# Kernel optimization log

Measured on AMD Instinct MI355X. Metric: run time of the kernel, lower is better.

## Reference

```python
import jax, jax.numpy as jnp
from jax import lax
import numpy as np

B, S, V, C, H, Z, NSTEP = 256, 128, 128, 16, 1024, 256, 128
VC = V * C


def _gru_cell(x, h, Wih, Whh, bih, bhh):
    # torch GRUCell: gates ordered r, z, n along rows of (3H, in)
    gi = x @ Wih.T + bih
    gh = h @ Whh.T + bhh
    ir, iz, inn = jnp.split(gi, 3, axis=-1)
    hr, hz, hn = jnp.split(gh, 3, axis=-1)
    r = jax.nn.sigmoid(ir + hr)
    zg = jax.nn.sigmoid(iz + hz)
    n = jnp.tanh(inn + r * hn)
    return (1.0 - zg) * n + zg * h


def setup_inputs() -> dict:
    key = jax.random.key(0)
    ks = jax.random.split(key, 32)
    sc = 0.05
    p = lambda k, shape: (jax.random.normal(k, shape, jnp.float32) * sc)
    inp = {
        "x": jax.random.normal(ks[0], (B, V, S), jnp.float32),
        "noise": jax.random.normal(ks[1], (B, Z), jnp.float32),
        "gruf_Wih": p(ks[2], (3 * H, V)), "gruf_Whh": p(ks[3], (3 * H, H)),
        "gruf_bih": p(ks[4], (3 * H,)), "gruf_bhh": p(ks[5], (3 * H,)),
        "grub_Wih": p(ks[6], (3 * H, V)), "grub_Whh": p(ks[7], (3 * H, H)),
        "grub_bih": p(ks[8], (3 * H,)), "grub_bhh": p(ks[9], (3 * H,)),
        "Wmu": p(ks[10], (Z, 2 * H)), "bmu": p(ks[11], (Z,)),
        "Wvar": p(ks[12], (Z, 2 * H)), "bvar": p(ks[13], (Z,)),
        "Winit": p(ks[14], (H, Z)), "binit": p(ks[15], (H,)),
        "c1_Wih": p(ks[16], (3 * H, Z + VC)), "c1_Whh": p(ks[17], (3 * H, H)),
        "c1_bih": p(ks[18], (3 * H,)), "c1_bhh": p(ks[19], (3 * H,)),
        "c2_Wih": p(ks[20], (3 * H, H)), "c2_Whh": p(ks[21], (3 * H, H)),
        "c2_bih": p(ks[22], (3 * H,)), "c2_bhh": p(ks[23], (3 * H,)),
        "Wout": p(ks[24], (VC, H)), "bout": p(ks[25], (VC,)),
    }
    return inp


def reference(x, noise, gruf_Wih, gruf_Whh, gruf_bih, gruf_bhh,
              grub_Wih, grub_Whh, grub_bih, grub_bhh,
              Wmu, bmu, Wvar, bvar, Winit, binit,
              c1_Wih, c1_Whh, c1_bih, c1_bhh,
              c2_Wih, c2_Whh, c2_bih, c2_bhh, Wout, bout):
    b = x.shape[0]
    xe = jnp.transpose(x, (0, 2, 1))           # (b, s, V)
    xt = jnp.swapaxes(xe, 0, 1)                # (s, b, V) time-major
    h0 = jnp.zeros((b, H), x.dtype)

    def step_f(h, xs):
        h2 = _gru_cell(xs, h, gruf_Wih, gruf_Whh, gruf_bih, gruf_bhh)
        return h2, None

    def step_b(h, xs):
        h2 = _gru_cell(xs, h, grub_Wih, grub_Whh, grub_bih, grub_bhh)
        return h2, None

    hf, _ = lax.scan(step_f, h0, xt)
    hb, _ = lax.scan(step_b, h0, xt[::-1])
    enc = jnp.concatenate([hf, hb], axis=-1)   # (b, 2H) = h_n transposed+flattened

    mu = enc @ Wmu.T + bmu
    var = jnp.exp(enc @ Wvar.T + bvar)         # Normal(mu, var): var is the scale
    z = mu + var * noise                       # rsample

    out0 = jnp.zeros((b, VC), x.dtype).at[:, -1].set(1.0)
    h1_0 = jnp.tanh(z @ Winit.T + binit)
    h2_0 = jnp.zeros((b, H), x.dtype)

    def dstep(carry, i):
        out, h1, h2 = carry
        inp = jnp.concatenate([out, z], axis=1)          # (b, VC + Z)
        h1n = _gru_cell(inp, h1, c1_Wih, c1_Whh, c1_bih, c1_bhh)
        h2_prev = jnp.where(i == 0, h1n, h2)             # hx[1] = hx[0] at step 0
        h2n = _gru_cell(h1n, h2_prev, c2_Wih, c2_Whh, c2_bih, c2_bhh)
        logits = h2n @ Wout.T + bout                     # (b, VC)
        ls = jax.nn.log_softmax(logits.reshape(b, C, V), axis=1).reshape(b, VC)
        # eval-mode _sampling: argmax -> one-hot (no gradient flows through it)
        out_n = jax.nn.one_hot(jnp.argmax(ls, axis=1), VC, dtype=ls.dtype)
        return (out_n, h1n, h2n), ls

    _, xs = lax.scan(dstep, (out0, h1_0, h2_0), jnp.arange(NSTEP))
    recon_seq = jnp.swapaxes(xs, 0, 1)                   # (b, n_step, VC)
    recon = jnp.transpose(recon_seq, (0, 2, 1)).reshape(b, C, V, NSTEP)
    return mu, var, z, recon
```

## Files before the change

kernel.cpp:

```cpp
#include <hip/hip_runtime.h>
#include <cstdint>
#include <cstddef>

typedef __attribute__((ext_vector_type(8))) short bf16x8;
typedef __attribute__((ext_vector_type(4))) float f32x4;
#define DEVI __device__ __forceinline__

constexpr int B = 256, S = 128, V = 128, C = 16, H = 1024, Z = 256, NSTEP = 128;
constexpr int VC = V * C, G3 = 3 * H;
constexpr size_t BVC = (size_t)B * VC;

typedef __attribute__((address_space(1))) const unsigned short* gas_p;
typedef __attribute__((address_space(3))) unsigned short* las_p;

DEVI unsigned short f2bf(float f){unsigned u=__float_as_uint(f);u+=0x7fffu+((u>>16)&1u);return (unsigned short)(u>>16);}
DEVI float sigm(float x){return 1.f/(1.f+expf(-x));}
DEVI f32x4 MFMA(bf16x8 a,bf16x8 b,f32x4 c){return __builtin_amdgcn_mfma_f32_16x16x32_bf16(a,b,c,0,0,0);}
DEVI void stage16(const unsigned short* g, unsigned short* l){__builtin_amdgcn_global_load_lds((gas_p)g,(las_p)l,16,0,0);}

DEVI unsigned long long ldc8(const void* p){return __hip_atomic_load((const unsigned long long*)p,__ATOMIC_RELAXED,__HIP_MEMORY_SCOPE_AGENT);}
DEVI void stc8(void* p, unsigned long long v){__hip_atomic_store((unsigned long long*)p,v,__ATOMIC_RELAXED,__HIP_MEMORY_SCOPE_AGENT);}
DEVI unsigned ldc4(const void* p){return __hip_atomic_load((const unsigned*)p,__ATOMIC_RELAXED,__HIP_MEMORY_SCOPE_AGENT);}
DEVI void stc4(void* p, unsigned v){__hip_atomic_store((unsigned*)p,v,__ATOMIC_RELAXED,__HIP_MEMORY_SCOPE_AGENT);}
DEVI bf16x8 ldfragc(const unsigned short* p){
  union{bf16x8 v;unsigned long long q[2];}u;
  u.q[0]=ldc8(p); u.q[1]=ldc8(p+4); return u.v;
}
DEVI unsigned long long pack4(float a,float b,float c,float d){
  return (unsigned long long)f2bf(a)|((unsigned long long)f2bf(b)<<16)|((unsigned long long)f2bf(c)<<32)|((unsigned long long)f2bf(d)<<48);
}
DEVI unsigned long long packf2(float a,float b){
  return (unsigned long long)__float_as_uint(a)|((unsigned long long)__float_as_uint(b)<<32);
}

DEVI void wv(int n){
  if(n==0)      asm volatile("s_waitcnt vmcnt(0)":::"memory");
  else if(n==4) asm volatile("s_waitcnt vmcnt(4)":::"memory");
  else if(n==8) asm volatile("s_waitcnt vmcnt(8)":::"memory");
  else if(n==10)asm volatile("s_waitcnt vmcnt(10)":::"memory");
  else if(n==12)asm volatile("s_waitcnt vmcnt(12)":::"memory");
  else if(n==16)asm volatile("s_waitcnt vmcnt(16)":::"memory");
  else if(n==20)asm volatile("s_waitcnt vmcnt(20)":::"memory");
}
DEVI void lg0(){asm volatile("s_waitcnt lgkmcnt(0)":::"memory");}
DEVI void cmb(){asm volatile("" ::: "memory");}
DEVI void drain_sync(){asm volatile("s_waitcnt vmcnt(0) lgkmcnt(0)":::"memory");__syncthreads();}

DEVI void waitflags(const unsigned* f,int base,int n,unsigned tgt){
  int lane=threadIdx.x&63;
  if (lane<n){
    const unsigned* a=&f[(size_t)(base+lane)<<4];
    while (ldc4(a)<tgt) __builtin_amdgcn_s_sleep(2);
  }
}
DEVI unsigned waitseq(const unsigned* f,int base,int n,unsigned tgt){
  int lane=threadIdx.x&63; unsigned v=tgt<<16;
  if (lane<n){
    const unsigned* a=&f[(size_t)(base+lane)<<4];
    v=ldc4(a);
    while ((v>>16)<tgt){__builtin_amdgcn_s_sleep(2); v=ldc4(a);}
  }
  return v;
}

#define LDHD(SRC,KT,Ha,Hb) { (Ha)=ldfragc((SRC)+(size_t)mrow*H+((KT)<<6)+(l4<<3)); (Hb)=ldfragc((SRC)+(size_t)mrow*H+((KT)<<6)+((4+l4)<<3)); cmb(); }

__global__ void k_cvt(const float* __restrict__ src, unsigned short* __restrict__ dst, int n){
  for (int i=blockIdx.x*256+threadIdx.x;i<n;i+=gridDim.x*256) dst[i]=f2bf(src[i]);
}

__global__ void k_xt(const float* __restrict__ x, unsigned short* __restrict__ xtb){
  __shared__ float tile[32][33];
  int sb=blockIdx.x*32, rb=blockIdx.y*32, tx=threadIdx.x, ty=threadIdx.y;
  for (int i=ty;i<32;i+=8) tile[i][tx]=x[(size_t)(rb+i)*S+sb+tx];
  __syncthreads();
  for (int i=ty;i<32;i+=8) xtb[(size_t)(sb+i)*(B*V)+rb+tx]=f2bf(tile[tx][i]);
}

__global__ void k_wt(const float* __restrict__ w, float* __restrict__ wt){
  __shared__ float tile[32][33];
  int vb=blockIdx.x*32, nb=blockIdx.y*32, tx=threadIdx.x, ty=threadIdx.y;
  for (int i=ty;i<32;i+=8) tile[i][tx]=w[(size_t)(nb+i)*(VC+Z)+vb+tx];
  __syncthreads();
  for (int i=ty;i<32;i+=8) wt[(size_t)(vb+i)*G3+nb+tx]=tile[tx][i];
}

__global__ __launch_bounds__(256) void k_mu_var_z(const float* __restrict__ hf,const float* __restrict__ hb,
    const float* __restrict__ Wmu,const float* __restrict__ bmu,
    const float* __restrict__ Wvar,const float* __restrict__ bvar,
    const float* __restrict__ noise,
    float* __restrict__ omu,float* __restrict__ ovar,float* __restrict__ oz,float* __restrict__ zws){
  __shared__ float e[2*H];
  int b=blockIdx.x, t=threadIdx.x;
  for (int i=0;i<2*H/256;++i){int k=t+i*256; e[k]=(k<H)?hf[b*H+k]:hb[b*H+k-H];}
  __syncthreads();
  const float* wm=Wmu+(size_t)t*2*H; const float* wv2=Wvar+(size_t)t*2*H;
  float am=bmu[t], av=bvar[t];
  for (int k=0;k<2*H;++k){am+=e[k]*wm[k];av+=e[k]*wv2[k];}
  float vv=expf(av), zz=am+vv*noise[b*Z+t];
  omu[b*Z+t]=am; ovar[b*Z+t]=vv; oz[b*Z+t]=zz; zws[b*Z+t]=zz;
}

__global__ void k_zpart(const float* __restrict__ z,const float* __restrict__ c1Wih,
                        const float* __restrict__ bih,float* __restrict__ zpart){
  int idx=blockIdx.x*256+threadIdx.x;
  int b=idx/G3, n=idx%G3;
  const float* w=c1Wih+(size_t)n*(VC+Z)+VC;
  const float* zr=z+b*Z;
  float a=bih[n];
  for (int k=0;k<Z;++k) a+=zr[k]*w[k];
  zpart[idx]=a;
}

__global__ void k_h1init(const float* __restrict__ z,const float* __restrict__ Winit,
                         const float* __restrict__ binit,
                         float* __restrict__ h1f,unsigned short* __restrict__ h1b,unsigned* __restrict__ F4){
  int idx=blockIdx.x*256+threadIdx.x;
  int b=idx>>10, jj=idx&(H-1);
  const float* w=Winit+(size_t)jj*Z;
  const float* zr=z+b*Z;
  float a=binit[jj];
  for (int k=0;k<Z;++k) a+=zr[k]*w[k];
  float t=tanhf(a);
  h1f[idx]=t; h1b[idx]=f2bf(t);
  if (idx<B) F4[(size_t)idx<<4]=(unsigned)(VC-1);
}

struct EncP {
  const unsigned short *xtb,*wihf,*whhf,*wihb,*whhb;
  const float *bihf,*bhhf,*bihb,*bhhb;
  unsigned short *hf0,*hf1,*hb0,*hb1;
  float *hf,*hb;
  unsigned* FE;
};

#define ENC_MM(DB,H0,H1) { const unsigned short* bb=lw+(DB)*6144; \
  _Pragma("unroll") for (int kf=0;kf<2;++kf){ \
    const int sw=(((kf<<2)+l4)^(l15&7))<<3; \
    bf16x8 hh=kf?(H1):(H0); \
    _Pragma("unroll") for (int nj=0;nj<2;++nj){ \
      const int ro=((nj<<4)+l15)*64+sw; \
      bf16x8 w0=*(const bf16x8*)&bb[ro]; \
      bf16x8 w1=*(const bf16x8*)&bb[2048+ro]; \
      bf16x8 w2=*(const bf16x8*)&bb[4096+ro]; \
      aR[nj]=MFMA(w0,hh,aR[nj]); aZ[nj]=MFMA(w1,hh,aZ[nj]); aNH[nj]=MFMA(w2,hh,aNH[nj]); } } }

#define ENC_MMX(DB,XKT) { const unsigned short* bb=lw+(DB)*6144; \
  _Pragma("unroll") for (int kf=0;kf<2;++kf){ \
    const int ch=(kf<<2)+l4; const int sw=(ch^(l15&7))<<3; \
    bf16x8 hh=*(const bf16x8*)&P.xtb[(size_t)xs*(B*V)+(size_t)mrow*V+((XKT)<<6)+(ch<<3)]; \
    _Pragma("unroll") for (int nj=0;nj<2;++nj){ \
      const int ro=((nj<<4)+l15)*64+sw; \
      bf16x8 w0=*(const bf16x8*)&bb[ro]; \
      bf16x8 w1=*(const bf16x8*)&bb[2048+ro]; \
      bf16x8 w2=*(const bf16x8*)&bb[4096+ro]; \
      aR[nj]=MFMA(w0,hh,aR[nj]); aZ[nj]=MFMA(w1,hh,aZ[nj]); aNX[nj]=MFMA(w2,hh,aNX[nj]); } } }

__global__ __launch_bounds__(256,1) void k_enc(EncP P){
  __shared__ unsigned short lws[49152];
  const int tid=threadIdx.x, wave=tid>>6, lane=tid&63;
  const int l15=lane&15, l4=lane>>4, l8r=lane>>3, l8c=lane&7;
  const int bid=blockIdx.x, xcd=bid&7, q=bid>>3;
  const int dir=q>>4, q2=q&15, jt=(q2&1)*8+xcd, mt=q2>>1;
  const int wm=(wave&1)*16, wn=(wave>>1)*32;
  const int gbase=(bid>>4)<<4;
  const unsigned short* wih=dir?P.wihb:P.wihf;
  const unsigned short* whh=dir?P.whhb:P.whhf;
  const float* bih=dir?P.bihb:P.bihf;
  const float* bhh=dir?P.bhhb:P.bhhf;
  unsigned short* hbuf[2]={dir?P.hb0:P.hf0, dir?P.hb1:P.hf1};
  unsigned short* lw=&lws[wave*12288];
  const int mrow=mt*32+wm+l15;

  f32x4 biR[2],biZ[2],biN[2],bhR[2],bhZ[2],bhN[2];
#pragma unroll
  for (int nj=0;nj<2;++nj){
    int j0=jt*64+wn+nj*16+(l4<<2);
    biR[nj]=*(const f32x4*)&bih[j0]; biZ[nj]=*(const f32x4*)&bih[H+j0]; biN[nj]=*(const f32x4*)&bih[2*H+j0];
    bhR[nj]=*(const f32x4*)&bhh[j0]; bhZ[nj]=*(const f32x4*)&bhh[H+j0]; bhN[nj]=*(const f32x4*)&bhh[2*H+j0];
  }
  float hreg[2][4]={};

  auto Wh=[&](int kt,int db){
    unsigned short* d=lw+db*6144;
#pragma unroll
    for (int g=0;g<3;++g)
#pragma unroll
      for (int i=0;i<4;++i)
        stage16(whh+(size_t)((g<<10)+jt*64+wn+i*8+l8r)*H+(kt<<6)+((l8c^l8r)<<3), d+(g*32+i*8)*64);
    cmb();
  };
  auto Wx=[&](int kt,int db){
    unsigned short* d=lw+db*6144;
#pragma unroll
    for (int g=0;g<3;++g)
#pragma unroll
      for (int i=0;i<4;++i)
        stage16(wih+(size_t)((g<<10)+jt*64+wn+i*8+l8r)*V+(kt<<6)+((l8c^l8r)<<3), d+(g*32+i*8)*64);
    cmb();
  };

  Wh(0,0); Wh(1,1);

  for (int s=0;s<S;++s){
    waitflags(P.FE,gbase,16,(unsigned)s);
    const unsigned short* hsrc=hbuf[s&1];
    unsigned short* hdst=hbuf[(s+1)&1];
    const int xs=dir?(S-1-s):s;
    bf16x8 hA0,hA1,hB0,hB1;
    f32x4 aR[2]={},aZ[2]={},aNH[2]={},aNX[2]={};
    LDHD(hsrc,0,hA0,hA1); LDHD(hsrc,1,hB0,hB1);
    wv(4);  ENC_MM(0,hA0,hA1); lg0(); Wh(2,0); LDHD(hsrc,2,hA0,hA1);
    for (int i=0;i<6;++i){
      wv(16); ENC_MM(1,hB0,hB1); lg0(); Wh(2*i+3,1); LDHD(hsrc,2*i+3,hB0,hB1);
      wv(16); ENC_MM(0,hA0,hA1); lg0(); Wh(2*i+4,0); LDHD(hsrc,2*i+4,hA0,hA1);
    }
    wv(16); ENC_MM(1,hB0,hB1); lg0(); Wh(15,1); LDHD(hsrc,15,hB0,hB1);
    wv(16); ENC_MM(0,hA0,hA1); lg0(); Wx(0,0);
    wv(12); ENC_MM(1,hB0,hB1); lg0(); Wx(1,1);
    wv(12); ENC_MMX(0,0); lg0();
    wv(0);  ENC_MMX(1,1); lg0();
#pragma unroll
    for (int nj=0;nj<2;++nj){
      int j0=jt*64+wn+nj*16+(l4<<2);
      float hv[4];
#pragma unroll
      for (int r=0;r<4;++r){
        float rg=sigm(aR[nj][r]+biR[nj][r]+bhR[nj][r]);
        float zg=sigm(aZ[nj][r]+biZ[nj][r]+bhZ[nj][r]);
        float nn=tanhf(aNX[nj][r]+biN[nj][r]+rg*(aNH[nj][r]+bhN[nj][r]));
        float hnew=(1.f-zg)*nn+zg*hreg[nj][r];
        hreg[nj][r]=hnew; hv[r]=hnew;
      }
      stc8(hdst+(size_t)mrow*H+j0, pack4(hv[0],hv[1],hv[2],hv[3]));
    }
    drain_sync();
    if (tid==0) stc4(&P.FE[(size_t)bid<<4],(unsigned)(s+1));
    Wh(0,0); Wh(1,1);
  }
  float* hout=dir?P.hb:P.hf;
#pragma unroll
  for (int nj=0;nj<2;++nj){
    int j0=jt*64+wn+nj*16+(l4<<2);
    f32x4 v; v[0]=hreg[nj][0];v[1]=hreg[nj][1];v[2]=hreg[nj][2];v[3]=hreg[nj][3];
    *(f32x4*)&hout[(size_t)mrow*H+j0]=v;
  }
}

struct DecP {
  unsigned short *h1b0,*h1b1,*h2b0,*h2b1;
  const unsigned short *w1hh,*w2ih,*w2hh,*wout;
  const float *bhh1,*bih2,*bhh2,*bout;
  const float *zpart,*WT,*h1f;
  float *logits,*lsbuf,*recon;
  unsigned *F1,*F2,*F3,*F4;
};

#define MM1(DB,H0,H1) { const unsigned short* bb=lw+(DB)*3072; \
  _Pragma("unroll") for (int kf=0;kf<2;++kf){ \
    const int sw=(((kf<<2)+l4)^(l15&7))<<3; const int ro=l15*64+sw; \
    bf16x8 w0=*(const bf16x8*)&bb[ro]; bf16x8 w1=*(const bf16x8*)&bb[1024+ro]; bf16x8 w2=*(const bf16x8*)&bb[2048+ro]; \
    bf16x8 hh=kf?(H1):(H0); \
    aR=MFMA(w0,hh,aR); aZ=MFMA(w1,hh,aZ); aN=MFMA(w2,hh,aN); } }

#define MM2(DB,A10,A11,A20,A21) { const unsigned short* bb=lw+(DB)*6144; \
  _Pragma("unroll") for (int kf=0;kf<2;++kf){ \
    const int sw=(((kf<<2)+l4)^(l15&7))<<3; const int ro=l15*64+sw; \
    bf16x8 wi0=*(const bf16x8*)&bb[ro];      bf16x8 wi1=*(const bf16x8*)&bb[1024+ro]; bf16x8 wi2=*(const bf16x8*)&bb[2048+ro]; \
    bf16x8 wh0=*(const bf16x8*)&bb[3072+ro]; bf16x8 wh1=*(const bf16x8*)&bb[4096+ro]; bf16x8 wh2=*(const bf16x8*)&bb[5120+ro]; \
    bf16x8 a1=kf?(A11):(A10), a2=kf?(A21):(A20); \
    aR=MFMA(wi0,a1,aR); aR=MFMA(wh0,a2,aR); \
    aZ=MFMA(wi1,a1,aZ); aZ=MFMA(wh1,a2,aZ); \
    aNI=MFMA(wi2,a1,aNI); aNH=MFMA(wh2,a2,aNH); } }

#define MM3(DB,H0,H1) { const unsigned short* bb=lw+(DB)*2048; \
  _Pragma("unroll") for (int kf=0;kf<2;++kf){ \
    const int sw=(((kf<<2)+l4)^(l15&7))<<3; \
    bf16x8 w0=*(const bf16x8*)&bb[l15*64+sw]; bf16x8 w1=*(const bf16x8*)&bb[(16+l15)*64+sw]; \
    bf16x8 hh=kf?(H1):(H0); \
    ac0=MFMA(w0,hh,ac0); ac1=MFMA(w1,hh,ac1); } }

__global__ __launch_bounds__(256,1) void k_dec(DecP P){
  __shared__ unsigned short lws[49152];
  __shared__ float sm_ls[VC];
  __shared__ float sm_rv[256];
  __shared__ int   sm_ri[256];
  const int tid=threadIdx.x, wave=tid>>6, lane=tid&63;
  const int l15=lane&15, l4=lane>>4, l8r=lane>>3, l8c=lane&7;
  const int bid=blockIdx.x, xcd=bid&7, q=bid>>3;
  const int jt=(q&3)*8+xcd, mt=q>>2;
  const int wm=(wave&1)*16, wn=(wave>>1)*16;
  const int wn3=(wave>>1)*32;
  const int base32=(bid>>5)<<5;
  unsigned short* lw=&lws[wave*12288];
  unsigned short* h1b[2]={P.h1b0,P.h1b1};
  unsigned short* h2b[2]={P.h2b0,P.h2b1};
  const int mrow=mt*32+wm+l15;
  const int j0=jt*32+wn+(l4<<2);

  f32x4 zR4=*(const f32x4*)&P.zpart[(size_t)mrow*G3+j0];
  f32x4 zZ4=*(const f32x4*)&P.zpart[(size_t)mrow*G3+H+j0];
  f32x4 zN4=*(const f32x4*)&P.zpart[(size_t)mrow*G3+2*H+j0];
  f32x4 b1R=*(const f32x4*)&P.bhh1[j0], b1Z=*(const f32x4*)&P.bhh1[H+j0], b1N=*(const f32x4*)&P.bhh1[2*H+j0];
  f32x4 c2Rv,c2Zv,biN2,bhN2;
  { f32x4 a=*(const f32x4*)&P.bih2[j0],   b2=*(const f32x4*)&P.bhh2[j0];   c2Rv=a+b2; }
  { f32x4 a=*(const f32x4*)&P.bih2[H+j0], b2=*(const f32x4*)&P.bhh2[H+j0]; c2Zv=a+b2; }
  biN2=*(const f32x4*)&P.bih2[2*H+j0]; bhN2=*(const f32x4*)&P.bhh2[2*H+j0];
  f32x4 bo0=*(const f32x4*)&P.bout[jt*64+wn3+(l4<<2)];
  f32x4 bo1=*(const f32x4*)&P.bout[jt*64+wn3+16+(l4<<2)];
  f32x4 h1i=*(const f32x4*)&P.h1f[(size_t)mrow*H+j0];
  float h1reg[4]={h1i[0],h1i[1],h1i[2],h1i[3]};
  float h2reg[4]={};

  auto W1i=[&](int kt,int db){
    unsigned short* d=lw+db*3072;
#pragma unroll
    for (int g=0;g<3;++g)
#pragma unroll
      for (int i=0;i<2;++i)
        stage16(P.w1hh+(size_t)((g<<10)+jt*32+wn+i*8+l8r)*H+(kt<<6)+((l8c^l8r)<<3), d+(g*16+i*8)*64);
    cmb();
  };
  auto W2i=[&](int kt,int db){
    unsigned short* d=lw+db*6144;
#pragma unroll
    for (int m=0;m<6;++m){
      const unsigned short* src=(m<3)?P.w2ih:P.w2hh;
      const int g=(m<3)?m:(m-3);
#pragma unroll
      for (int i=0;i<2;++i)
        stage16(src+(size_t)((g<<10)+jt*32+wn+i*8+l8r)*H+(kt<<6)+((l8c^l8r)<<3), d+(m*16+i*8)*64);
    }
    cmb();
  };
  auto W3i=[&](int kt,int db){
    unsigned short* d=lw+db*2048;
#pragma unroll
    for (int i=0;i<4;++i)
      stage16(P.wout+(size_t)(jt*64+wn3+i*8+l8r)*H+(kt<<6)+((l8c^l8r)<<3), d+i*8*64);
    cmb();
  };

  W1i(0,0); W1i(1,1);

  for (int t=0;t<NSTEP;++t){
    const int cur=t&1, nxt=cur^1;
    {
      unsigned fv=waitseq(P.F4,base32,32,(unsigned)t);
      int idxm=(int)(__shfl(fv,wm+l15)&0xffffu);
      const float* wtr=P.WT+(size_t)idxm*G3;
      f32x4 wR=*(const f32x4*)&wtr[j0], wZ=*(const f32x4*)&wtr[H+j0], wN=*(const f32x4*)&wtr[2*H+j0];
      const unsigned short* h1src=h1b[cur];
      bf16x8 hA0,hA1,hB0,hB1;
      f32x4 aR={},aZ={},aN={};
      LDHD(h1src,0,hA0,hA1); LDHD(h1src,1,hB0,hB1);
      wv(4);  MM1(0,hA0,hA1); lg0(); W1i(2,0); LDHD(h1src,2,hA0,hA1);
      for (int i=0;i<6;++i){
        wv(10); MM1(1,hB0,hB1); lg0(); W1i(2*i+3,1); LDHD(h1src,2*i+3,hB0,hB1);
        wv(10); MM1(0,hA0,hA1); lg0(); W1i(2*i+4,0); LDHD(h1src,2*i+4,hA0,hA1);
      }
      wv(10); MM1(1,hB0,hB1); lg0(); W1i(15,1); LDHD(h1src,15,hB0,hB1);
      wv(10); MM1(0,hA0,hA1); lg0();
      wv(0);  MM1(1,hB0,hB1); lg0();
      float hv[4];
#pragma unroll
      for (int r=0;r<4;++r){
        float rg=sigm(zR4[r]+wR[r]+aR[r]+b1R[r]);
        float zg=sigm(zZ4[r]+wZ[r]+aZ[r]+b1Z[r]);
        float nn=tanhf(zN4[r]+wN[r]+rg*(aN[r]+b1N[r]));
        float hnew=(1.f-zg)*nn+zg*h1reg[r];
        h1reg[r]=hnew; hv[r]=hnew;
      }
      stc8(h1b[nxt]+(size_t)mrow*H+j0, pack4(hv[0],hv[1],hv[2],hv[3]));
    }
    drain_sync();
    if (tid==0) stc4(&P.F1[(size_t)bid<<4],(unsigned)(t+1));
    W2i(0,0); W2i(1,1);
    waitflags(P.F1,base32,32,(unsigned)(t+1));
    {
      const unsigned short* s1=h1b[nxt];
      const unsigned short* s2=(t==0)?h1b[nxt]:h2b[cur];
      bf16x8 xA0,xA1,yA0,yA1,xB0,xB1,yB0,yB1;
      f32x4 aR={},aZ={},aNI={},aNH={};
      LDHD(s1,0,xA0,xA1); LDHD(s2,0,yA0,yA1); LDHD(s1,1,xB0,xB1); LDHD(s2,1,yB0,yB1);
      wv(8);  MM2(0,xA0,xA1,yA0,yA1); lg0(); W2i(2,0); LDHD(s1,2,xA0,xA1); LDHD(s2,2,yA0,yA1);
      for (int i=0;i<6;++i){
        wv(20); MM2(1,xB0,xB1,yB0,yB1); lg0(); W2i(2*i+3,1); LDHD(s1,2*i+3,xB0,xB1); LDHD(s2,2*i+3,yB0,yB1);
        wv(20); MM2(0,xA0,xA1,yA0,yA1); lg0(); W2i(2*i+4,0); LDHD(s1,2*i+4,xA0,xA1); LDHD(s2,2*i+4,yA0,yA1);
      }
      wv(20); MM2(1,xB0,xB1,yB0,yB1); lg0(); W2i(15,1); LDHD(s1,15,xB0,xB1); LDHD(s2,15,yB0,yB1);
      wv(20); MM2(0,xA0,xA1,yA0,yA1); lg0();
      wv(0);  MM2(1,xB0,xB1,yB0,yB1); lg0();
      float hv[4];
#pragma unroll
      for (int r=0;r<4;++r){
        float rg=sigm(aR[r]+c2Rv[r]);
        float zg=sigm(aZ[r]+c2Zv[r]);
        float nn=tanhf(aNI[r]+biN2[r]+rg*(aNH[r]+bhN2[r]));
        float hp=(t==0)?h1reg[r]:h2reg[r];
        float hnew=(1.f-zg)*nn+zg*hp;
        h2reg[r]=hnew; hv[r]=hnew;
      }
      stc8(h2b[nxt]+(size_t)mrow*H+j0, pack4(hv[0],hv[1],hv[2],hv[3]));
    }
    drain_sync();
    if (tid==0) stc4(&P.F2[(size_t)bid<<4],(unsigned)(t+1));
    W3i(0,0); W3i(1,1);
    waitflags(P.F2,base32,32,(unsigned)(t+1));
    {
      const unsigned short* hs=h2b[nxt];
      bf16x8 hA0,hA1,hB0,hB1;
      f32x4 ac0={},ac1={};
      LDHD(hs,0,hA0,hA1); LDHD(hs,1,hB0,hB1);
      wv(4); MM3(0,hA0,hA1); lg0(); W3i(2,0); LDHD(hs,2,hA0,hA1);
      for (int i=0;i<6;++i){
        wv(8); MM3(1,hB0,hB1); lg0(); W3i(2*i+3,1); LDHD(hs,2*i+3,hB0,hB1);
        wv(8); MM3(0,hA0,hA1); lg0(); W3i(2*i+4,0); LDHD(hs,2*i+4,hA0,hA1);
      }
      wv(8); MM3(1,hB0,hB1); lg0(); W3i(15,1); LDHD(hs,15,hB0,hB1);
      wv(8); MM3(0,hA0,hA1); lg0();
      wv(0); MM3(1,hB0,hB1); lg0();
      int n0=jt*64+wn3+(l4<<2);
      stc8(&P.logits[(size_t)mrow*VC+n0],    packf2(ac0[0]+bo0[0],ac0[1]+bo0[1]));
      stc8(&P.logits[(size_t)mrow*VC+n0+2],  packf2(ac0[2]+bo0[2],ac0[3]+bo0[3]));
      stc8(&P.logits[(size_t)mrow*VC+n0+16], packf2(ac1[0]+bo1[0],ac1[1]+bo1[1]));
      stc8(&P.logits[(size_t)mrow*VC+n0+18], packf2(ac1[2]+bo1[2],ac1[3]+bo1[3]));
    }
    drain_sync();
    if (tid==0) stc4(&P.F3[(size_t)bid<<4],(unsigned)(t+1));
    waitflags(P.F3,base32,32,(unsigned)(t+1));
    int ri0;
    {
      const int b=bid;
#pragma unroll
      for (int i=0;i<4;++i){
        unsigned long long qq=ldc8(&P.logits[(size_t)b*VC+tid*8+i*2]);
        sm_ls[tid*8+i*2]  =__uint_as_float((unsigned)qq);
        sm_ls[tid*8+i*2+1]=__uint_as_float((unsigned)(qq>>32));
      }
      __syncthreads();
      if (tid<V){
        float mx=-1e30f;
        for (int c=0;c<C;++c) mx=fmaxf(mx,sm_ls[c*V+tid]);
        float sum=0.f;
        for (int c=0;c<C;++c) sum+=expf(sm_ls[c*V+tid]-mx);
        float lse=mx+logf(sum);
        for (int c=0;c<C;++c) sm_ls[c*V+tid]-=lse;
      }
      __syncthreads();
      float bv=-1e30f; int bi=0;
#pragma unroll
      for (int i=0;i<VC/256;++i){
        int n=i*256+tid; float v=sm_ls[n];
        if (v>bv){bv=v;bi=n;}
      }
      sm_rv[tid]=bv; sm_ri[tid]=bi;
      __syncthreads();
      for (int s2=128;s2>0;s2>>=1){
        if (tid<s2){
          float v2=sm_rv[tid+s2]; int i2=sm_ri[tid+s2];
          if (v2>sm_rv[tid]||(v2==sm_rv[tid]&&i2<sm_ri[tid])){sm_rv[tid]=v2;sm_ri[tid]=i2;}
        }
        __syncthreads();
      }
      ri0=sm_ri[0];
      float* dst=P.lsbuf+(size_t)(t&15)*BVC+(size_t)bid*VC;
#pragma unroll
      for (int i=0;i<4;++i)
        stc8(&dst[tid*8+i*2], packf2(sm_ls[tid*8+i*2],sm_ls[tid*8+i*2+1]));
    }
    drain_sync();
    if (tid==0) stc4(&P.F4[(size_t)bid<<4], ((unsigned)(t+1)<<16)|(unsigned)ri0);
    W1i(0,0); W1i(1,1);
    if ((t&15)==15){
      const int t0=t-15;
      const size_t e0=((size_t)bid*256+tid)*8;
#pragma unroll
      for (int pe=0;pe<4;++pe){
        float va[16],vb[16];
#pragma unroll
        for (int j2=0;j2<16;++j2){
          unsigned long long qq=ldc8(&P.lsbuf[(size_t)j2*BVC+e0+pe*2]);
          va[j2]=__uint_as_float((unsigned)qq); vb[j2]=__uint_as_float((unsigned)(qq>>32));
        }
        float* d0=&P.recon[(e0+pe*2)*NSTEP+t0];
        float* d1=&P.recon[(e0+pe*2+1)*NSTEP+t0];
#pragma unroll
        for (int k=0;k<16;++k){ d0[k]=va[k]; d1[k]=vb[k]; }
      }
    }
  }
}

extern "C" void kernel_launch(void* const* d_in, const int* in_sizes, int n_in,
                              void* d_out, int out_size, void* d_ws, size_t ws_size,
                              hipStream_t stream) {
  const float* x        = (const float*)d_in[0];
  const float* noise    = (const float*)d_in[1];
  const float* gruf_Wih = (const float*)d_in[2];
  const float* gruf_Whh = (const float*)d_in[3];
  const float* gruf_bih = (const float*)d_in[4];
  const float* gruf_bhh = (const float*)d_in[5];
  const float* grub_Wih = (const float*)d_in[6];
  const float* grub_Whh = (const float*)d_in[7];
  const float* grub_bih = (const float*)d_in[8];
  const float* grub_bhh = (const float*)d_in[9];
  const float* Wmu      = (const float*)d_in[10];
  const float* bmu      = (const float*)d_in[11];
  const float* Wvar     = (const float*)d_in[12];
  const float* bvar     = (const float*)d_in[13];
  const float* Winit    = (const float*)d_in[14];
  const float* binit    = (const float*)d_in[15];
  const float* c1_Wih   = (const float*)d_in[16];
  const float* c1_Whh   = (const float*)d_in[17];
  const float* c1_bih   = (const float*)d_in[18];
  const float* c1_bhh   = (const float*)d_in[19];
  const float* c2_Wih   = (const float*)d_in[20];
  const float* c2_Whh   = (const float*)d_in[21];
  const float* c2_bih   = (const float*)d_in[22];
  const float* c2_bhh   = (const float*)d_in[23];
  const float* Wout     = (const float*)d_in[24];
  const float* bout     = (const float*)d_in[25];

  float* omu = (float*)d_out;
  float* ovar = omu + B*Z;
  float* oz = ovar + B*Z;
  float* orecon = oz + B*Z;

  char* p = (char*)d_ws;
  auto carve = [&](size_t bytes){ char* r = p; p += (bytes+255)&~(size_t)255; return r; };
  unsigned short* wihf_b  = (unsigned short*)carve((size_t)G3*V*2);
  unsigned short* whhf_b  = (unsigned short*)carve((size_t)G3*H*2);
  unsigned short* wihb_b  = (unsigned short*)carve((size_t)G3*V*2);
  unsigned short* whhb_b  = (unsigned short*)carve((size_t)G3*H*2);
  unsigned short* wc1hh_b = (unsigned short*)carve((size_t)G3*H*2);
  unsigned short* wc2ih_b = (unsigned short*)carve((size_t)G3*H*2);
  unsigned short* wc2hh_b = (unsigned short*)carve((size_t)G3*H*2);
  unsigned short* wout_b  = (unsigned short*)carve((size_t)VC*H*2);
  unsigned short* xtb     = (unsigned short*)carve((size_t)S*B*V*2);
  unsigned short* hf0     = (unsigned short*)carve((size_t)B*H*2);
  unsigned short* hf1     = (unsigned short*)carve((size_t)B*H*2);
  unsigned short* hb0     = (unsigned short*)carve((size_t)B*H*2);
  unsigned short* hb1     = (unsigned short*)carve((size_t)B*H*2);
  unsigned short* h1b0    = (unsigned short*)carve((size_t)B*H*2);
  unsigned short* h1b1    = (unsigned short*)carve((size_t)B*H*2);
  unsigned short* h2b0    = (unsigned short*)carve((size_t)B*H*2);
  unsigned short* h2b1    = (unsigned short*)carve((size_t)B*H*2);
  float* WT     = (float*)carve((size_t)VC*G3*4);
  float* zpart  = (float*)carve((size_t)B*G3*4);
  float* hf     = (float*)carve((size_t)B*H*4);
  float* hb     = (float*)carve((size_t)B*H*4);
  float* h1f    = (float*)carve((size_t)B*H*4);
  float* zws    = (float*)carve((size_t)B*Z*4);
  float* logits = (float*)carve((size_t)B*VC*4);
  float* lsbuf  = (float*)carve((size_t)16*BVC*4);
  unsigned* FE  = (unsigned*)carve(16384);
  unsigned* F1  = (unsigned*)carve(16384);
  unsigned* F2  = (unsigned*)carve(16384);
  unsigned* F3  = (unsigned*)carve(16384);
  unsigned* F4  = (unsigned*)carve(16384);

  dim3 blk(256);
  auto cvt=[&](const float* s, unsigned short* d, int n){
    int nb=(n+255)/256; if (nb>2048) nb=2048;
    k_cvt<<<nb,blk,0,stream>>>(s,d,n);
  };
  cvt(gruf_Wih,wihf_b,G3*V);
  cvt(gruf_Whh,whhf_b,G3*H);
  cvt(grub_Wih,wihb_b,G3*V);
  cvt(grub_Whh,whhb_b,G3*H);
  cvt(c1_Whh,wc1hh_b,G3*H);
  cvt(c2_Wih,wc2ih_b,G3*H);
  cvt(c2_Whh,wc2hh_b,G3*H);
  cvt(Wout,wout_b,VC*H);
  k_xt<<<dim3(S/32,(B*V)/32),dim3(32,8),0,stream>>>(x,xtb);
  k_wt<<<dim3(VC/32,G3/32),dim3(32,8),0,stream>>>(c1_Wih,WT);
  hipMemsetAsync(hf0,0,(size_t)B*H*2,stream);
  hipMemsetAsync(hb0,0,(size_t)B*H*2,stream);
  hipMemsetAsync(FE,0,5*16384,stream);

  EncP ep;
  ep.xtb=xtb; ep.wihf=wihf_b; ep.whhf=whhf_b; ep.wihb=wihb_b; ep.whhb=whhb_b;
  ep.bihf=gruf_bih; ep.bhhf=gruf_bhh; ep.bihb=grub_bih; ep.bhhb=grub_bhh;
  ep.hf0=hf0; ep.hf1=hf1; ep.hb0=hb0; ep.hb1=hb1;
  ep.hf=hf; ep.hb=hb; ep.FE=FE;
  k_enc<<<256,blk,0,stream>>>(ep);

  k_mu_var_z<<<B,blk,0,stream>>>(hf,hb,Wmu,bmu,Wvar,bvar,noise,omu,ovar,oz,zws);
  k_zpart<<<B*G3/256,blk,0,stream>>>(zws,c1_Wih,c1_bih,zpart);
  k_h1init<<<B*H/256,blk,0,stream>>>(zws,Winit,binit,h1f,h1b0,F4);

  DecP dp;
  dp.h1b0=h1b0; dp.h1b1=h1b1; dp.h2b0=h2b0; dp.h2b1=h2b1;
  dp.w1hh=wc1hh_b; dp.w2ih=wc2ih_b; dp.w2hh=wc2hh_b; dp.wout=wout_b;
  dp.bhh1=c1_bhh; dp.bih2=c2_bih; dp.bhh2=c2_bhh; dp.bout=bout;
  dp.zpart=zpart; dp.WT=WT; dp.h1f=h1f;
  dp.logits=logits; dp.lsbuf=lsbuf; dp.recon=orecon;
  dp.F1=F1; dp.F2=F2; dp.F3=F3; dp.F4=F4;
  k_dec<<<256,blk,0,stream>>>(dp);
}
```

Measured before the change: 9.678 ms.

## Restructure encoder and decoder GRU kernels around LDS-staged hidden panels

```diff
diff --git a/kernel.cpp b/kernel.cpp
--- a/kernel.cpp
+++ b/kernel.cpp
@@ -22,10 +22,6 @@
 DEVI void stc8(void* p, unsigned long long v){__hip_atomic_store((unsigned long long*)p,v,__ATOMIC_RELAXED,__HIP_MEMORY_SCOPE_AGENT);}
 DEVI unsigned ldc4(const void* p){return __hip_atomic_load((const unsigned*)p,__ATOMIC_RELAXED,__HIP_MEMORY_SCOPE_AGENT);}
 DEVI void stc4(void* p, unsigned v){__hip_atomic_store((unsigned*)p,v,__ATOMIC_RELAXED,__HIP_MEMORY_SCOPE_AGENT);}
-DEVI bf16x8 ldfragc(const unsigned short* p){
-  union{bf16x8 v;unsigned long long q[2];}u;
-  u.q[0]=ldc8(p); u.q[1]=ldc8(p+4); return u.v;
-}
 DEVI unsigned long long pack4(float a,float b,float c,float d){
   return (unsigned long long)f2bf(a)|((unsigned long long)f2bf(b)<<16)|((unsigned long long)f2bf(c)<<32)|((unsigned long long)f2bf(d)<<48);
 }
@@ -35,35 +31,30 @@
 
 DEVI void wv(int n){
   if(n==0)      asm volatile("s_waitcnt vmcnt(0)":::"memory");
+  else if(n==2) asm volatile("s_waitcnt vmcnt(2)":::"memory");
+  else if(n==3) asm volatile("s_waitcnt vmcnt(3)":::"memory");
   else if(n==4) asm volatile("s_waitcnt vmcnt(4)":::"memory");
-  else if(n==8) asm volatile("s_waitcnt vmcnt(8)":::"memory");
-  else if(n==10)asm volatile("s_waitcnt vmcnt(10)":::"memory");
-  else if(n==12)asm volatile("s_waitcnt vmcnt(12)":::"memory");
-  else if(n==16)asm volatile("s_waitcnt vmcnt(16)":::"memory");
-  else if(n==20)asm volatile("s_waitcnt vmcnt(20)":::"memory");
+  else if(n==6) asm volatile("s_waitcnt vmcnt(6)":::"memory");
 }
 DEVI void lg0(){asm volatile("s_waitcnt lgkmcnt(0)":::"memory");}
 DEVI void cmb(){asm volatile("" ::: "memory");}
-DEVI void drain_sync(){asm volatile("s_waitcnt vmcnt(0) lgkmcnt(0)":::"memory");__syncthreads();}
 
 DEVI void waitflags(const unsigned* f,int base,int n,unsigned tgt){
   int lane=threadIdx.x&63;
   if (lane<n){
     const unsigned* a=&f[(size_t)(base+lane)<<4];
-    while (ldc4(a)<tgt) __builtin_amdgcn_s_sleep(2);
+    while (ldc4(a)<tgt) __builtin_amdgcn_s_sleep(1);
   }
 }
 DEVI unsigned waitseq(const unsigned* f,int base,int n,unsigned tgt){
-  int lane=threadIdx.x&63; unsigned v=tgt<<16;
+  int lane=threadIdx.x&63; unsigned v=tgt<<24;
   if (lane<n){
     const unsigned* a=&f[(size_t)(base+lane)<<4];
     v=ldc4(a);
-    while ((v>>16)<tgt){__builtin_amdgcn_s_sleep(2); v=ldc4(a);}
+    while ((v>>24)<tgt){__builtin_amdgcn_s_sleep(1); v=ldc4(a);}
   }
   return v;
 }
-
-#define LDHD(SRC,KT,Ha,Hb) { (Ha)=ldfragc((SRC)+(size_t)mrow*H+((KT)<<6)+(l4<<3)); (Hb)=ldfragc((SRC)+(size_t)mrow*H+((KT)<<6)+((4+l4)<<3)); cmb(); }
 
 __global__ void k_cvt(const float* __restrict__ src, unsigned short* __restrict__ dst, int n){
   for (int i=blockIdx.x*256+threadIdx.x;i<n;i+=gridDim.x*256) dst[i]=f2bf(src[i]);
@@ -123,7 +114,7 @@
   for (int k=0;k<Z;++k) a+=zr[k]*w[k];
   float t=tanhf(a);
   h1f[idx]=t; h1b[idx]=f2bf(t);
-  if (idx<B) F4[(size_t)idx<<4]=(unsigned)(VC-1);
+  if (idx<128) F4[(size_t)idx<<4]=((unsigned)(VC-1)<<12)|(unsigned)(VC-1);
 }
 
 struct EncP {
@@ -134,117 +125,105 @@
   unsigned* FE;
 };
 
-#define ENC_MM(DB,H0,H1) { const unsigned short* bb=lw+(DB)*6144; \
-  _Pragma("unroll") for (int kf=0;kf<2;++kf){ \
-    const int sw=(((kf<<2)+l4)^(l15&7))<<3; \
-    bf16x8 hh=kf?(H1):(H0); \
-    _Pragma("unroll") for (int nj=0;nj<2;++nj){ \
-      const int ro=((nj<<4)+l15)*64+sw; \
-      bf16x8 w0=*(const bf16x8*)&bb[ro]; \
-      bf16x8 w1=*(const bf16x8*)&bb[2048+ro]; \
-      bf16x8 w2=*(const bf16x8*)&bb[4096+ro]; \
-      aR[nj]=MFMA(w0,hh,aR[nj]); aZ[nj]=MFMA(w1,hh,aZ[nj]); aNH[nj]=MFMA(w2,hh,aNH[nj]); } } }
-
-#define ENC_MMX(DB,XKT) { const unsigned short* bb=lw+(DB)*6144; \
-  _Pragma("unroll") for (int kf=0;kf<2;++kf){ \
-    const int ch=(kf<<2)+l4; const int sw=(ch^(l15&7))<<3; \
-    bf16x8 hh=*(const bf16x8*)&P.xtb[(size_t)xs*(B*V)+(size_t)mrow*V+((XKT)<<6)+(ch<<3)]; \
-    _Pragma("unroll") for (int nj=0;nj<2;++nj){ \
-      const int ro=((nj<<4)+l15)*64+sw; \
-      bf16x8 w0=*(const bf16x8*)&bb[ro]; \
-      bf16x8 w1=*(const bf16x8*)&bb[2048+ro]; \
-      bf16x8 w2=*(const bf16x8*)&bb[4096+ro]; \
-      aR[nj]=MFMA(w0,hh,aR[nj]); aZ[nj]=MFMA(w1,hh,aZ[nj]); aNX[nj]=MFMA(w2,hh,aNX[nj]); } } }
-
-__global__ __launch_bounds__(256,1) void k_enc(EncP P){
-  __shared__ unsigned short lws[49152];
+__global__ __launch_bounds__(512,1) void k_enc(EncP P){
+  __shared__ unsigned short L[55296];
   const int tid=threadIdx.x, wave=tid>>6, lane=tid&63;
-  const int l15=lane&15, l4=lane>>4, l8r=lane>>3, l8c=lane&7;
-  const int bid=blockIdx.x, xcd=bid&7, q=bid>>3;
-  const int dir=q>>4, q2=q&15, jt=(q2&1)*8+xcd, mt=q2>>1;
-  const int wm=(wave&1)*16, wn=(wave>>1)*32;
-  const int gbase=(bid>>4)<<4;
+  const int l15=lane&15, l4=lane>>4;
+  const int r8=lane>>2, pcl=lane&3;
+  const int csw=(pcl-(r8>>1))&3;
+  const int bid=blockIdx.x, jt=bid&7, mt=(bid>>3)&15, dir=bid>>7;
+  const int g8=bid&~7;
   const unsigned short* wih=dir?P.wihb:P.wihf;
   const unsigned short* whh=dir?P.whhb:P.whhf;
   const float* bih=dir?P.bihb:P.bihf;
   const float* bhh=dir?P.bhhb:P.bhhf;
   unsigned short* hbuf[2]={dir?P.hb0:P.hf0, dir?P.hb1:P.hf1};
-  unsigned short* lw=&lws[wave*12288];
-  const int mrow=mt*32+wm+l15;
-
-  f32x4 biR[2],biZ[2],biN[2],bhR[2],bhZ[2],bhN[2];
-#pragma unroll
-  for (int nj=0;nj<2;++nj){
-    int j0=jt*64+wn+nj*16+(l4<<2);
-    biR[nj]=*(const f32x4*)&bih[j0]; biZ[nj]=*(const f32x4*)&bih[H+j0]; biN[nj]=*(const f32x4*)&bih[2*H+j0];
-    bhR[nj]=*(const f32x4*)&bhh[j0]; bhZ[nj]=*(const f32x4*)&bhh[H+j0]; bhN[nj]=*(const f32x4*)&bhh[2*H+j0];
-  }
-  float hreg[2][4]={};
-
-  auto Wh=[&](int kt,int db){
-    unsigned short* d=lw+db*6144;
-#pragma unroll
-    for (int g=0;g<3;++g)
-#pragma unroll
-      for (int i=0;i<4;++i)
-        stage16(whh+(size_t)((g<<10)+jt*64+wn+i*8+l8r)*H+(kt<<6)+((l8c^l8r)<<3), d+(g*32+i*8)*64);
+  const int m=mt*16+l15;
+  const int j0=jt*128+wave*16+(l4<<2);
+  const int WBe=18432;
+
+  f32x4 cR,cZ,bNi,bNh;
+  { f32x4 a=*(const f32x4*)&bih[j0],   b2=*(const f32x4*)&bhh[j0];   cR=a+b2; }
+  { f32x4 a=*(const f32x4*)&bih[H+j0], b2=*(const f32x4*)&bhh[H+j0]; cZ=a+b2; }
+  bNi=*(const f32x4*)&bih[2*H+j0]; bNh=*(const f32x4*)&bhh[2*H+j0];
+  float hreg[4]={};
+
+  auto W=[&](int kt,int buf){
+    unsigned short* d=&L[WBe + wave*4608 + buf*1536];
+    if (kt<32){
+#pragma unroll
+      for (int g=0;g<3;++g)
+        stage16(whh + (size_t)((g<<10)+jt*128+wave*16+r8)*H + (kt<<5) + csw*8, d+(g<<9));
+    } else {
+      int kx=kt-32;
+#pragma unroll
+      for (int g=0;g<3;++g)
+        stage16(wih + (size_t)((g<<10)+jt*128+wave*16+r8)*V + (kx<<5) + csw*8, d+(g<<9));
+    }
     cmb();
   };
-  auto Wx=[&](int kt,int db){
-    unsigned short* d=lw+db*6144;
-#pragma unroll
-    for (int g=0;g<3;++g)
-#pragma unroll
-      for (int i=0;i<4;++i)
-        stage16(wih+(size_t)((g<<10)+jt*64+wn+i*8+l8r)*V+(kt<<6)+((l8c^l8r)<<3), d+(g*32+i*8)*64);
-    cmb();
-  };
-
-  Wh(0,0); Wh(1,1);
 
   for (int s=0;s<S;++s){
-    waitflags(P.FE,gbase,16,(unsigned)s);
-    const unsigned short* hsrc=hbuf[s&1];
-    unsigned short* hdst=hbuf[(s+1)&1];
-    const int xs=dir?(S-1-s):s;
-    bf16x8 hA0,hA1,hB0,hB1;
-    f32x4 aR[2]={},aZ[2]={},aNH[2]={},aNX[2]={};
-    LDHD(hsrc,0,hA0,hA1); LDHD(hsrc,1,hB0,hB1);
-    wv(4);  ENC_MM(0,hA0,hA1); lg0(); Wh(2,0); LDHD(hsrc,2,hA0,hA1);
-    for (int i=0;i<6;++i){
-      wv(16); ENC_MM(1,hB0,hB1); lg0(); Wh(2*i+3,1); LDHD(hsrc,2*i+3,hB0,hB1);
-      wv(16); ENC_MM(0,hA0,hA1); lg0(); Wh(2*i+4,0); LDHD(hsrc,2*i+4,hA0,hA1);
-    }
-    wv(16); ENC_MM(1,hB0,hB1); lg0(); Wh(15,1); LDHD(hsrc,15,hB0,hB1);
-    wv(16); ENC_MM(0,hA0,hA1); lg0(); Wx(0,0);
-    wv(12); ENC_MM(1,hB0,hB1); lg0(); Wx(1,1);
-    wv(12); ENC_MMX(0,0); lg0();
-    wv(0);  ENC_MMX(1,1); lg0();
-#pragma unroll
-    for (int nj=0;nj<2;++nj){
-      int j0=jt*64+wn+nj*16+(l4<<2);
-      float hv[4];
-#pragma unroll
-      for (int r=0;r<4;++r){
-        float rg=sigm(aR[nj][r]+biR[nj][r]+bhR[nj][r]);
-        float zg=sigm(aZ[nj][r]+biZ[nj][r]+bhZ[nj][r]);
-        float nn=tanhf(aNX[nj][r]+biN[nj][r]+rg*(aNH[nj][r]+bhN[nj][r]));
-        float hnew=(1.f-zg)*nn+zg*hreg[nj][r];
-        hreg[nj][r]=hnew; hv[r]=hnew;
-      }
-      stc8(hdst+(size_t)mrow*H+j0, pack4(hv[0],hv[1],hv[2],hv[3]));
-    }
-    drain_sync();
+    waitflags(P.FE,g8,8,(unsigned)s);
+    {
+      const unsigned short* hs=hbuf[s&1] + (size_t)mt*16*H;
+      unsigned long long q[8];
+#pragma unroll
+      for (int i=0;i<8;++i) q[i]=ldc8(hs + (i*512+tid)*4);
+#pragma unroll
+      for (int i=0;i<8;++i){
+        int e=i*512+tid, row=e>>8, u=e&255, c=u>>1;
+        int ph=(c&~7)|((c+(row>>1))&7);
+        *(unsigned long long*)&L[row*1024 + ph*8 + (u&1)*4]=q[i];
+      }
+      const int xs=dir?(S-1-s):s;
+      if (tid<256){
+        int row=tid>>4, c=tid&15;
+        uint4 v=*(const uint4*)&P.xtb[(size_t)xs*(B*V)+(size_t)(mt*16+row)*V+(c<<3)];
+        int ph=(c&~7)|((c+(row>>1))&7);
+        *(uint4*)&L[16384 + row*128 + ph*8]=v;
+      }
+    }
+    __syncthreads();
+    W(0,0); W(1,1); W(2,2);
+    f32x4 aR={},aZ={},aNH={},aNX={};
+    int buf=0;
+    for (int kt=0;kt<36;++kt){
+      if (kt<34) wv(6); else if (kt==34) wv(3); else wv(0);
+      bf16x8 b;
+      if (kt<32){
+        int c=(kt<<2)+l4, ph=(c&~7)|((c+(l15>>1))&7);
+        b=*(const bf16x8*)&L[l15*1024 + ph*8];
+      } else {
+        int c=((kt-32)<<2)+l4, ph=(c&~7)|((c+(l15>>1))&7);
+        b=*(const bf16x8*)&L[16384 + l15*128 + ph*8];
+      }
+      int ab=WBe + wave*4608 + buf*1536 + l15*32 + (((l4+(l15>>1))&3)<<3);
+      bf16x8 a0=*(const bf16x8*)&L[ab];
+      bf16x8 a1=*(const bf16x8*)&L[ab+512];
+      bf16x8 a2=*(const bf16x8*)&L[ab+1024];
+      aR=MFMA(a0,b,aR); aZ=MFMA(a1,b,aZ);
+      if (kt<32) aNH=MFMA(a2,b,aNH); else aNX=MFMA(a2,b,aNX);
+      lg0();
+      if (kt<33) W(kt+3,buf);
+      buf=(buf==2)?0:buf+1;
+    }
+    float hv[4];
+#pragma unroll
+    for (int r=0;r<4;++r){
+      float rg=sigm(aR[r]+cR[r]);
+      float zg=sigm(aZ[r]+cZ[r]);
+      float nn=tanhf(aNX[r]+bNi[r]+rg*(aNH[r]+bNh[r]));
+      float hnew=(1.f-zg)*nn+zg*hreg[r];
+      hreg[r]=hnew; hv[r]=hnew;
+    }
+    stc8(hbuf[(s+1)&1] + (size_t)m*H + j0, pack4(hv[0],hv[1],hv[2],hv[3]));
+    wv(0); __syncthreads();
     if (tid==0) stc4(&P.FE[(size_t)bid<<4],(unsigned)(s+1));
-    Wh(0,0); Wh(1,1);
   }
   float* hout=dir?P.hb:P.hf;
-#pragma unroll
-  for (int nj=0;nj<2;++nj){
-    int j0=jt*64+wn+nj*16+(l4<<2);
-    f32x4 v; v[0]=hreg[nj][0];v[1]=hreg[nj][1];v[2]=hreg[nj][2];v[3]=hreg[nj][3];
-    *(f32x4*)&hout[(size_t)mrow*H+j0]=v;
-  }
+  f32x4 v; v[0]=hreg[0];v[1]=hreg[1];v[2]=hreg[2];v[3]=hreg[3];
+  *(f32x4*)&hout[(size_t)m*H+j0]=v;
 }
 
 struct DecP {
@@ -256,112 +235,103 @@
   unsigned *F1,*F2,*F3,*F4;
 };
 
-#define MM1(DB,H0,H1) { const unsigned short* bb=lw+(DB)*3072; \
-  _Pragma("unroll") for (int kf=0;kf<2;++kf){ \
-    const int sw=(((kf<<2)+l4)^(l15&7))<<3; const int ro=l15*64+sw; \
-    bf16x8 w0=*(const bf16x8*)&bb[ro]; bf16x8 w1=*(const bf16x8*)&bb[1024+ro]; bf16x8 w2=*(const bf16x8*)&bb[2048+ro]; \
-    bf16x8 hh=kf?(H1):(H0); \
-    aR=MFMA(w0,hh,aR); aZ=MFMA(w1,hh,aZ); aN=MFMA(w2,hh,aN); } }
-
-#define MM2(DB,A10,A11,A20,A21) { const unsigned short* bb=lw+(DB)*6144; \
-  _Pragma("unroll") for (int kf=0;kf<2;++kf){ \
-    const int sw=(((kf<<2)+l4)^(l15&7))<<3; const int ro=l15*64+sw; \
-    bf16x8 wi0=*(const bf16x8*)&bb[ro];      bf16x8 wi1=*(const bf16x8*)&bb[1024+ro]; bf16x8 wi2=*(const bf16x8*)&bb[2048+ro]; \
-    bf16x8 wh0=*(const bf16x8*)&bb[3072+ro]; bf16x8 wh1=*(const bf16x8*)&bb[4096+ro]; bf16x8 wh2=*(const bf16x8*)&bb[5120+ro]; \
-    bf16x8 a1=kf?(A11):(A10), a2=kf?(A21):(A20); \
-    aR=MFMA(wi0,a1,aR); aR=MFMA(wh0,a2,aR); \
-    aZ=MFMA(wi1,a1,aZ); aZ=MFMA(wh1,a2,aZ); \
-    aNI=MFMA(wi2,a1,aNI); aNH=MFMA(wh2,a2,aNH); } }
-
-#define MM3(DB,H0,H1) { const unsigned short* bb=lw+(DB)*2048; \
-  _Pragma("unroll") for (int kf=0;kf<2;++kf){ \
-    const int sw=(((kf<<2)+l4)^(l15&7))<<3; \
-    bf16x8 w0=*(const bf16x8*)&bb[l15*64+sw]; bf16x8 w1=*(const bf16x8*)&bb[(16+l15)*64+sw]; \
-    bf16x8 hh=kf?(H1):(H0); \
-    ac0=MFMA(w0,hh,ac0); ac1=MFMA(w1,hh,ac1); } }
-
-__global__ __launch_bounds__(256,1) void k_dec(DecP P){
-  __shared__ unsigned short lws[49152];
-  __shared__ float sm_ls[VC];
-  __shared__ float sm_rv[256];
-  __shared__ int   sm_ri[256];
+__global__ __launch_bounds__(512,1) void k_dec(DecP P){
+  __shared__ unsigned short L[69632];
   const int tid=threadIdx.x, wave=tid>>6, lane=tid&63;
-  const int l15=lane&15, l4=lane>>4, l8r=lane>>3, l8c=lane&7;
-  const int bid=blockIdx.x, xcd=bid&7, q=bid>>3;
-  const int jt=(q&3)*8+xcd, mt=q>>2;
-  const int wm=(wave&1)*16, wn=(wave>>1)*16;
-  const int wn3=(wave>>1)*32;
-  const int base32=(bid>>5)<<5;
-  unsigned short* lw=&lws[wave*12288];
+  const int l15=lane&15, l4=lane>>4;
+  const int r8=lane>>2, pcl=lane&3;
+  const int csw=(pcl-(r8>>1))&3;
+  const int bid=blockIdx.x, jb=bid&7, mt=bid>>3;
+  const int g8=bid&~7;
+  const int WB=32768;
   unsigned short* h1b[2]={P.h1b0,P.h1b1};
   unsigned short* h2b[2]={P.h2b0,P.h2b1};
-  const int mrow=mt*32+wm+l15;
-  const int j0=jt*32+wn+(l4<<2);
-
-  f32x4 zR4=*(const f32x4*)&P.zpart[(size_t)mrow*G3+j0];
-  f32x4 zZ4=*(const f32x4*)&P.zpart[(size_t)mrow*G3+H+j0];
-  f32x4 zN4=*(const f32x4*)&P.zpart[(size_t)mrow*G3+2*H+j0];
+  const int m=mt*16+l15;
+  const int j0=jb*128+wave*16+(l4<<2);
+  const int n0=jb*256+wave*32+(l4<<2);
+
+  f32x4 zR4=*(const f32x4*)&P.zpart[(size_t)m*G3+j0];
+  f32x4 zZ4=*(const f32x4*)&P.zpart[(size_t)m*G3+H+j0];
+  f32x4 zN4=*(const f32x4*)&P.zpart[(size_t)m*G3+2*H+j0];
   f32x4 b1R=*(const f32x4*)&P.bhh1[j0], b1Z=*(const f32x4*)&P.bhh1[H+j0], b1N=*(const f32x4*)&P.bhh1[2*H+j0];
-  f32x4 c2Rv,c2Zv,biN2,bhN2;
-  { f32x4 a=*(const f32x4*)&P.bih2[j0],   b2=*(const f32x4*)&P.bhh2[j0];   c2Rv=a+b2; }
-  { f32x4 a=*(const f32x4*)&P.bih2[H+j0], b2=*(const f32x4*)&P.bhh2[H+j0]; c2Zv=a+b2; }
+  f32x4 c2R,c2Z,biN2,bhN2;
+  { f32x4 a=*(const f32x4*)&P.bih2[j0],   b2=*(const f32x4*)&P.bhh2[j0];   c2R=a+b2; }
+  { f32x4 a=*(const f32x4*)&P.bih2[H+j0], b2=*(const f32x4*)&P.bhh2[H+j0]; c2Z=a+b2; }
   biN2=*(const f32x4*)&P.bih2[2*H+j0]; bhN2=*(const f32x4*)&P.bhh2[2*H+j0];
-  f32x4 bo0=*(const f32x4*)&P.bout[jt*64+wn3+(l4<<2)];
-  f32x4 bo1=*(const f32x4*)&P.bout[jt*64+wn3+16+(l4<<2)];
-  f32x4 h1i=*(const f32x4*)&P.h1f[(size_t)mrow*H+j0];
+  f32x4 bo0=*(const f32x4*)&P.bout[n0];
+  f32x4 bo1=*(const f32x4*)&P.bout[n0+16];
+  f32x4 h1i=*(const f32x4*)&P.h1f[(size_t)m*H+j0];
   float h1reg[4]={h1i[0],h1i[1],h1i[2],h1i[3]};
   float h2reg[4]={};
 
-  auto W1i=[&](int kt,int db){
-    unsigned short* d=lw+db*3072;
+  auto loadPanel=[&](const unsigned short* src,int base){
+    const unsigned short* hs=src + (size_t)mt*16*H;
+    unsigned long long q[8];
+#pragma unroll
+    for (int i=0;i<8;++i) q[i]=ldc8(hs + (i*512+tid)*4);
+#pragma unroll
+    for (int i=0;i<8;++i){
+      int e=i*512+tid, row=e>>8, u=e&255, c=u>>1;
+      int ph=(c&~7)|((c+(row>>1))&7);
+      *(unsigned long long*)&L[base + row*1024 + ph*8 + (u&1)*4]=q[i];
+    }
+  };
+  auto PFRAG=[&](int base,int kt)->bf16x8{
+    int c=(kt<<2)+l4, ph=(c&~7)|((c+(l15>>1))&7);
+    return *(const bf16x8*)&L[base + l15*1024 + ph*8];
+  };
+  auto W1=[&](int kt,int buf){
+    unsigned short* d=&L[WB + wave*4608 + buf*1536];
 #pragma unroll
     for (int g=0;g<3;++g)
-#pragma unroll
-      for (int i=0;i<2;++i)
-        stage16(P.w1hh+(size_t)((g<<10)+jt*32+wn+i*8+l8r)*H+(kt<<6)+((l8c^l8r)<<3), d+(g*16+i*8)*64);
+      stage16(P.w1hh + (size_t)((g<<10)+jb*128+wave*16+r8)*H + (kt<<5) + csw*8, d+(g<<9));
     cmb();
   };
-  auto W2i=[&](int kt,int db){
-    unsigned short* d=lw+db*6144;
-#pragma unroll
-    for (int m=0;m<6;++m){
-      const unsigned short* src=(m<3)?P.w2ih:P.w2hh;
-      const int g=(m<3)?m:(m-3);
-#pragma unroll
-      for (int i=0;i<2;++i)
-        stage16(src+(size_t)((g<<10)+jt*32+wn+i*8+l8r)*H+(kt<<6)+((l8c^l8r)<<3), d+(m*16+i*8)*64);
-    }
+  auto W2=[&](int kt,int buf){
+    unsigned short* d=&L[WB + wave*4608 + buf*1536];
+    const unsigned short* src=(kt<32)?P.w2ih:P.w2hh;
+    int ko=(kt<32)?(kt<<5):((kt-32)<<5);
+#pragma unroll
+    for (int g=0;g<3;++g)
+      stage16(src + (size_t)((g<<10)+jb*128+wave*16+r8)*H + ko + csw*8, d+(g<<9));
     cmb();
   };
-  auto W3i=[&](int kt,int db){
-    unsigned short* d=lw+db*2048;
-#pragma unroll
-    for (int i=0;i<4;++i)
-      stage16(P.wout+(size_t)(jt*64+wn3+i*8+l8r)*H+(kt<<6)+((l8c^l8r)<<3), d+i*8*64);
+  auto W3=[&](int kt,int buf){
+    unsigned short* d=&L[WB + wave*3072 + buf*1024];
+#pragma unroll
+    for (int nt=0;nt<2;++nt)
+      stage16(P.wout + (size_t)(jb*256+wave*32+(nt<<4)+r8)*H + (kt<<5) + csw*8, d+(nt<<9));
     cmb();
   };
 
-  W1i(0,0); W1i(1,1);
+  loadPanel(h1b[0],0);
 
   for (int t=0;t<NSTEP;++t){
     const int cur=t&1, nxt=cur^1;
     {
-      unsigned fv=waitseq(P.F4,base32,32,(unsigned)t);
-      int idxm=(int)(__shfl(fv,wm+l15)&0xffffu);
+      unsigned fv=waitseq(P.F4,g8,8,(unsigned)t);
+      unsigned vv=__shfl(fv,(l15>>1));
+      int idxm=(int)((vv>>(12*(l15&1)))&0xfffu);
       const float* wtr=P.WT+(size_t)idxm*G3;
-      f32x4 wR=*(const f32x4*)&wtr[j0], wZ=*(const f32x4*)&wtr[H+j0], wN=*(const f32x4*)&wtr[2*H+j0];
-      const unsigned short* h1src=h1b[cur];
-      bf16x8 hA0,hA1,hB0,hB1;
+      f32x4 wR=*(const f32x4*)&wtr[j0];
+      f32x4 wZ=*(const f32x4*)&wtr[H+j0];
+      f32x4 wN=*(const f32x4*)&wtr[2*H+j0];
+      __syncthreads();
+      W1(0,0); W1(1,1); W1(2,2);
       f32x4 aR={},aZ={},aN={};
-      LDHD(h1src,0,hA0,hA1); LDHD(h1src,1,hB0,hB1);
-      wv(4);  MM1(0,hA0,hA1); lg0(); W1i(2,0); LDHD(h1src,2,hA0,hA1);
-      for (int i=0;i<6;++i){
-        wv(10); MM1(1,hB0,hB1); lg0(); W1i(2*i+3,1); LDHD(h1src,2*i+3,hB0,hB1);
-        wv(10); MM1(0,hA0,hA1); lg0(); W1i(2*i+4,0); LDHD(h1src,2*i+4,hA0,hA1);
-      }
-      wv(10); MM1(1,hB0,hB1); lg0(); W1i(15,1); LDHD(h1src,15,hB0,hB1);
-      wv(10); MM1(0,hA0,hA1); lg0();
-      wv(0);  MM1(1,hB0,hB1); lg0();
+      int buf=0;
+      for (int kt=0;kt<32;++kt){
+        if (kt<30) wv(6); else if (kt==30) wv(3); else wv(0);
+        bf16x8 b=PFRAG(0,kt);
+        int ab=WB + wave*4608 + buf*1536 + l15*32 + (((l4+(l15>>1))&3)<<3);
+        bf16x8 a0=*(const bf16x8*)&L[ab];
+        bf16x8 a1=*(const bf16x8*)&L[ab+512];
+        bf16x8 a2=*(const bf16x8*)&L[ab+1024];
+        aR=MFMA(a0,b,aR); aZ=MFMA(a1,b,aZ); aN=MFMA(a2,b,aN);
+        lg0();
+        if (kt<29) W1(kt+3,buf);
+        buf=(buf==2)?0:buf+1;
+      }
       float hv[4];
 #pragma unroll
       for (int r=0;r<4;++r){
@@ -371,124 +341,135 @@
         float hnew=(1.f-zg)*nn+zg*h1reg[r];
         h1reg[r]=hnew; hv[r]=hnew;
       }
-      stc8(h1b[nxt]+(size_t)mrow*H+j0, pack4(hv[0],hv[1],hv[2],hv[3]));
-    }
-    drain_sync();
-    if (tid==0) stc4(&P.F1[(size_t)bid<<4],(unsigned)(t+1));
-    W2i(0,0); W2i(1,1);
-    waitflags(P.F1,base32,32,(unsigned)(t+1));
+      stc8(h1b[nxt]+(size_t)m*H+j0, pack4(hv[0],hv[1],hv[2],hv[3]));
+      wv(0); __syncthreads();
+      if (tid==0) stc4(&P.F1[(size_t)bid<<4],(unsigned)(t+1));
+    }
     {
-      const unsigned short* s1=h1b[nxt];
-      const unsigned short* s2=(t==0)?h1b[nxt]:h2b[cur];
-      bf16x8 xA0,xA1,yA0,yA1,xB0,xB1,yB0,yB1;
+      waitflags(P.F1,g8,8,(unsigned)(t+1));
+      loadPanel(h1b[nxt],0);
+      loadPanel((t==0)?h1b[nxt]:h2b[cur],16384);
+      __syncthreads();
+      W2(0,0); W2(1,1); W2(2,2);
       f32x4 aR={},aZ={},aNI={},aNH={};
-      LDHD(s1,0,xA0,xA1); LDHD(s2,0,yA0,yA1); LDHD(s1,1,xB0,xB1); LDHD(s2,1,yB0,yB1);
-      wv(8);  MM2(0,xA0,xA1,yA0,yA1); lg0(); W2i(2,0); LDHD(s1,2,xA0,xA1); LDHD(s2,2,yA0,yA1);
-      for (int i=0;i<6;++i){
-        wv(20); MM2(1,xB0,xB1,yB0,yB1); lg0(); W2i(2*i+3,1); LDHD(s1,2*i+3,xB0,xB1); LDHD(s2,2*i+3,yB0,yB1);
-        wv(20); MM2(0,xA0,xA1,yA0,yA1); lg0(); W2i(2*i+4,0); LDHD(s1,2*i+4,xA0,xA1); LDHD(s2,2*i+4,yA0,yA1);
-      }
-      wv(20); MM2(1,xB0,xB1,yB0,yB1); lg0(); W2i(15,1); LDHD(s1,15,xB0,xB1); LDHD(s2,15,yB0,yB1);
-      wv(20); MM2(0,xA0,xA1,yA0,yA1); lg0();
-      wv(0);  MM2(1,xB0,xB1,yB0,yB1); lg0();
+      int buf=0;
+      for (int kt=0;kt<64;++kt){
+        if (kt<62) wv(6); else if (kt==62) wv(3); else wv(0);
+        bf16x8 b=(kt<32)?PFRAG(0,kt):PFRAG(16384,kt-32);
+        int ab=WB + wave*4608 + buf*1536 + l15*32 + (((l4+(l15>>1))&3)<<3);
+        bf16x8 a0=*(const bf16x8*)&L[ab];
+        bf16x8 a1=*(const bf16x8*)&L[ab+512];
+        bf16x8 a2=*(const bf16x8*)&L[ab+1024];
+        aR=MFMA(a0,b,aR); aZ=MFMA(a1,b,aZ);
+        if (kt<32) aNI=MFMA(a2,b,aNI); else aNH=MFMA(a2,b,aNH);
+        lg0();
+        if (kt<61) W2(kt+3,buf);
+        buf=(buf==2)?0:buf+1;
+      }
       float hv[4];
 #pragma unroll
       for (int r=0;r<4;++r){
-        float rg=sigm(aR[r]+c2Rv[r]);
-        float zg=sigm(aZ[r]+c2Zv[r]);
+        float rg=sigm(aR[r]+c2R[r]);
+        float zg=sigm(aZ[r]+c2Z[r]);
         float nn=tanhf(aNI[r]+biN2[r]+rg*(aNH[r]+bhN2[r]));
         float hp=(t==0)?h1reg[r]:h2reg[r];
         float hnew=(1.f-zg)*nn+zg*hp;
         h2reg[r]=hnew; hv[r]=hnew;
       }
-      stc8(h2b[nxt]+(size_t)mrow*H+j0, pack4(hv[0],hv[1],hv[2],hv[3]));
-    }
-    drain_sync();
-    if (tid==0) stc4(&P.F2[(size_t)bid<<4],(unsigned)(t+1));
-    W3i(0,0); W3i(1,1);
-    waitflags(P.F2,base32,32,(unsigned)(t+1));
+      stc8(h2b[nxt]+(size_t)m*H+j0, pack4(hv[0],hv[1],hv[2],hv[3]));
+      wv(0); __syncthreads();
+      if (tid==0) stc4(&P.F2[(size_t)bid<<4],(unsigned)(t+1));
+    }
     {
-      const unsigned short* hs=h2b[nxt];
-      bf16x8 hA0,hA1,hB0,hB1;
+      waitflags(P.F2,g8,8,(unsigned)(t+1));
+      loadPanel(h2b[nxt],0);
+      __syncthreads();
+      W3(0,0); W3(1,1); W3(2,2);
       f32x4 ac0={},ac1={};
-      LDHD(hs,0,hA0,hA1); LDHD(hs,1,hB0,hB1);
-      wv(4); MM3(0,hA0,hA1); lg0(); W3i(2,0); LDHD(hs,2,hA0,hA1);
-      for (int i=0;i<6;++i){
-        wv(8); MM3(1,hB0,hB1); lg0(); W3i(2*i+3,1); LDHD(hs,2*i+3,hB0,hB1);
-        wv(8); MM3(0,hA0,hA1); lg0(); W3i(2*i+4,0); LDHD(hs,2*i+4,hA0,hA1);
-      }
-      wv(8); MM3(1,hB0,hB1); lg0(); W3i(15,1); LDHD(hs,15,hB0,hB1);
-      wv(8); MM3(0,hA0,hA1); lg0();
-      wv(0); MM3(1,hB0,hB1); lg0();
-      int n0=jt*64+wn3+(l4<<2);
-      stc8(&P.logits[(size_t)mrow*VC+n0],    packf2(ac0[0]+bo0[0],ac0[1]+bo0[1]));
-      stc8(&P.logits[(size_t)mrow*VC+n0+2],  packf2(ac0[2]+bo0[2],ac0[3]+bo0[3]));
-      stc8(&P.logits[(size_t)mrow*VC+n0+16], packf2(ac1[0]+bo1[0],ac1[1]+bo1[1]));
-      stc8(&P.logits[(size_t)mrow*VC+n0+18], packf2(ac1[2]+bo1[2],ac1[3]+bo1[3]));
-    }
-    drain_sync();
-    if (tid==0) stc4(&P.F3[(size_t)bid<<4],(unsigned)(t+1));
-    waitflags(P.F3,base32,32,(unsigned)(t+1));
-    int ri0;
+      int buf=0;
+      for (int kt=0;kt<32;++kt){
+        if (kt<30) wv(4); else if (kt==30) wv(2); else wv(0);
+        bf16x8 b=PFRAG(0,kt);
+        int ab=WB + wave*3072 + buf*1024 + l15*32 + (((l4+(l15>>1))&3)<<3);
+        bf16x8 a0=*(const bf16x8*)&L[ab];
+        bf16x8 a1=*(const bf16x8*)&L[ab+512];
+        ac0=MFMA(a0,b,ac0); ac1=MFMA(a1,b,ac1);
+        lg0();
+        if (kt<29) W3(kt+3,buf);
+        buf=(buf==2)?0:buf+1;
+      }
+      stc8(&P.logits[(size_t)m*VC+n0],    packf2(ac0[0]+bo0[0],ac0[1]+bo0[1]));
+      stc8(&P.logits[(size_t)m*VC+n0+2],  packf2(ac0[2]+bo0[2],ac0[3]+bo0[3]));
+      stc8(&P.logits[(size_t)m*VC+n0+16], packf2(ac1[0]+bo1[0],ac1[1]+bo1[1]));
+      stc8(&P.logits[(size_t)m*VC+n0+18], packf2(ac1[2]+bo1[2],ac1[3]+bo1[3]));
+      wv(0); __syncthreads();
+      if (tid==0) stc4(&P.F3[(size_t)bid<<4],(unsigned)(t+1));
+    }
     {
-      const int b=bid;
+      waitflags(P.F3,g8,8,(unsigned)(t+1));
+      float* SM=(float*)&L[WB];
+      const int row=tid>>8, t2=tid&255;
+      const int b4=bid*2+row;
 #pragma unroll
       for (int i=0;i<4;++i){
-        unsigned long long qq=ldc8(&P.logits[(size_t)b*VC+tid*8+i*2]);
-        sm_ls[tid*8+i*2]  =__uint_as_float((unsigned)qq);
-        sm_ls[tid*8+i*2+1]=__uint_as_float((unsigned)(qq>>32));
+        unsigned long long q=ldc8(&P.logits[(size_t)b4*VC + t2*8 + i*2]);
+        SM[row*2048+t2*8+i*2]  =__uint_as_float((unsigned)q);
+        SM[row*2048+t2*8+i*2+1]=__uint_as_float((unsigned)(q>>32));
       }
       __syncthreads();
-      if (tid<V){
+      if (t2<V){
         float mx=-1e30f;
-        for (int c=0;c<C;++c) mx=fmaxf(mx,sm_ls[c*V+tid]);
-        float sum=0.f;
-        for (int c=0;c<C;++c) sum+=expf(sm_ls[c*V+tid]-mx);
-        float lse=mx+logf(sum);
-        for (int c=0;c<C;++c) sm_ls[c*V+tid]-=lse;
+        for (int c=0;c<C;++c) mx=fmaxf(mx,SM[row*2048+c*V+t2]);
+        float su=0.f;
+        for (int c=0;c<C;++c) su+=expf(SM[row*2048+c*V+t2]-mx);
+        float lse=mx+logf(su);
+        for (int c=0;c<C;++c) SM[row*2048+c*V+t2]-=lse;
       }
       __syncthreads();
       float bv=-1e30f; int bi=0;
 #pragma unroll
-      for (int i=0;i<VC/256;++i){
-        int n=i*256+tid; float v=sm_ls[n];
+      for (int i=0;i<8;++i){
+        int n=t2*8+i; float v=SM[row*2048+n];
         if (v>bv){bv=v;bi=n;}
       }
-      sm_rv[tid]=bv; sm_ri[tid]=bi;
+      float* RV=SM+4096; int* RI=(int*)(SM+4608);
+      RV[row*256+t2]=bv; RI[row*256+t2]=bi;
       __syncthreads();
       for (int s2=128;s2>0;s2>>=1){
-        if (tid<s2){
-          float v2=sm_rv[tid+s2]; int i2=sm_ri[tid+s2];
-          if (v2>sm_rv[tid]||(v2==sm_rv[tid]&&i2<sm_ri[tid])){sm_rv[tid]=v2;sm_ri[tid]=i2;}
+        if (t2<s2){
+          float v2=RV[row*256+t2+s2]; int i2=RI[row*256+t2+s2];
+          if (v2>RV[row*256+t2]||(v2==RV[row*256+t2]&&i2<RI[row*256+t2])){RV[row*256+t2]=v2;RI[row*256+t2]=i2;}
         }
         __syncthreads();
       }
-      ri0=sm_ri[0];
-      float* dst=P.lsbuf+(size_t)(t&15)*BVC+(size_t)bid*VC;
+      float* dst=P.lsbuf+(size_t)(t&15)*BVC+(size_t)b4*VC;
 #pragma unroll
       for (int i=0;i<4;++i)
-        stc8(&dst[tid*8+i*2], packf2(sm_ls[tid*8+i*2],sm_ls[tid*8+i*2+1]));
-    }
-    drain_sync();
-    if (tid==0) stc4(&P.F4[(size_t)bid<<4], ((unsigned)(t+1)<<16)|(unsigned)ri0);
-    W1i(0,0); W1i(1,1);
+        stc8(&dst[t2*8+i*2], packf2(SM[row*2048+t2*8+i*2],SM[row*2048+t2*8+i*2+1]));
+      wv(0); __syncthreads();
+      if (tid==0){
+        unsigned i0=(unsigned)RI[0], i1=(unsigned)RI[256];
+        stc4(&P.F4[(size_t)bid<<4], ((unsigned)(t+1)<<24)|(i1<<12)|i0);
+      }
+    }
     if ((t&15)==15){
       const int t0=t-15;
-      const size_t e0=((size_t)bid*256+tid)*8;
-#pragma unroll
-      for (int pe=0;pe<4;++pe){
+      const size_t e0=(size_t)bid*4096 + (size_t)tid*8;
+#pragma unroll
+      for (int pp=0;pp<4;++pp){
         float va[16],vb[16];
 #pragma unroll
         for (int j2=0;j2<16;++j2){
-          unsigned long long qq=ldc8(&P.lsbuf[(size_t)j2*BVC+e0+pe*2]);
-          va[j2]=__uint_as_float((unsigned)qq); vb[j2]=__uint_as_float((unsigned)(qq>>32));
+          unsigned long long q=ldc8(&P.lsbuf[(size_t)j2*BVC + e0 + pp*2]);
+          va[j2]=__uint_as_float((unsigned)q); vb[j2]=__uint_as_float((unsigned)(q>>32));
         }
-        float* d0=&P.recon[(e0+pe*2)*NSTEP+t0];
-        float* d1=&P.recon[(e0+pe*2+1)*NSTEP+t0];
+        float* d0=&P.recon[(e0+pp*2)*NSTEP+t0];
+        float* d1=&P.recon[(e0+pp*2+1)*NSTEP+t0];
 #pragma unroll
         for (int k=0;k<16;++k){ d0[k]=va[k]; d1[k]=vb[k]; }
       }
     }
+    loadPanel(h1b[nxt],0);
   }
 }
 
@@ -555,15 +536,15 @@
   float* logits = (float*)carve((size_t)B*VC*4);
   float* lsbuf  = (float*)carve((size_t)16*BVC*4);
   unsigned* FE  = (unsigned*)carve(16384);
-  unsigned* F1  = (unsigned*)carve(16384);
-  unsigned* F2  = (unsigned*)carve(16384);
-  unsigned* F3  = (unsigned*)carve(16384);
-  unsigned* F4  = (unsigned*)carve(16384);
-
-  dim3 blk(256);
+  unsigned* F1  = (unsigned*)carve(8192);
+  unsigned* F2  = (unsigned*)carve(8192);
+  unsigned* F3  = (unsigned*)carve(8192);
+  unsigned* F4  = (unsigned*)carve(8192);
+
+  dim3 b256(256);
   auto cvt=[&](const float* s, unsigned short* d, int n){
     int nb=(n+255)/256; if (nb>2048) nb=2048;
-    k_cvt<<<nb,blk,0,stream>>>(s,d,n);
+    k_cvt<<<nb,b256,0,stream>>>(s,d,n);
   };
   cvt(gruf_Wih,wihf_b,G3*V);
   cvt(gruf_Whh,whhf_b,G3*H);
@@ -577,18 +558,18 @@
   k_wt<<<dim3(VC/32,G3/32),dim3(32,8),0,stream>>>(c1_Wih,WT);
   hipMemsetAsync(hf0,0,(size_t)B*H*2,stream);
   hipMemsetAsync(hb0,0,(size_t)B*H*2,stream);
-  hipMemsetAsync(FE,0,5*16384,stream);
+  hipMemsetAsync(FE,0,16384+4*8192,stream);
 
   EncP ep;
   ep.xtb=xtb; ep.wihf=wihf_b; ep.whhf=whhf_b; ep.wihb=wihb_b; ep.whhb=whhb_b;
   ep.bihf=gruf_bih; ep.bhhf=gruf_bhh; ep.bihb=grub_bih; ep.bhhb=grub_bhh;
   ep.hf0=hf0; ep.hf1=hf1; ep.hb0=hb0; ep.hb1=hb1;
   ep.hf=hf; ep.hb=hb; ep.FE=FE;
-  k_enc<<<256,blk,0,stream>>>(ep);
-
-  k_mu_var_z<<<B,blk,0,stream>>>(hf,hb,Wmu,bmu,Wvar,bvar,noise,omu,ovar,oz,zws);
-  k_zpart<<<B*G3/256,blk,0,stream>>>(zws,c1_Wih,c1_bih,zpart);
-  k_h1init<<<B*H/256,blk,0,stream>>>(zws,Winit,binit,h1f,h1b0,F4);
+  k_enc<<<256,dim3(512),0,stream>>>(ep);
+
+  k_mu_var_z<<<B,b256,0,stream>>>(hf,hb,Wmu,bmu,Wvar,bvar,noise,omu,ovar,oz,zws);
+  k_zpart<<<B*G3/256,b256,0,stream>>>(zws,c1_Wih,c1_bih,zpart);
+  k_h1init<<<B*H/256,b256,0,stream>>>(zws,Winit,binit,h1f,h1b0,F4);
 
   DecP dp;
   dp.h1b0=h1b0; dp.h1b1=h1b1; dp.h2b0=h2b0; dp.h2b1=h2b1;
@@ -597,5 +578,5 @@
   dp.zpart=zpart; dp.WT=WT; dp.h1f=h1f;
   dp.logits=logits; dp.lsbuf=lsbuf; dp.recon=orecon;
   dp.F1=F1; dp.F2=F2; dp.F3=F3; dp.F4=F4;
-  k_dec<<<256,blk,0,stream>>>(dp);
-}
+  k_dec<<<128,dim3(512),0,stream>>>(dp);
+}
```

Measured after the change: 9.206 ms. 4.9% less time.
